# Kernel tuning notes

Hardware: AMD Instinct MI355X
Metric: run time of the kernel (lower is better)

The kernel has to match this reference:

```python
import jax, jax.numpy as jnp
import numpy as np

H, DST, DCONV, EXP = 640, 16, 4, 2
DIN = H * EXP          # 1280
DTR = -(-H // 16)      # 40
EPS = 1e-6


def rmsnorm(x, w):
    rms = jnp.sqrt(jnp.mean(x * x, axis=-1, keepdims=True) + EPS)
    return x / rms * w


def bitlinear(x, w, nw):
    # RMSNorm -> ternary weight quant + int8 activation quant (STE)
    x = rmsnorm(x, nw)
    alpha = jnp.maximum(jnp.mean(jnp.abs(w)), 1e-10)
    wq = jnp.clip(jnp.round(w / alpha), -1.0, 1.0)
    wq = w + jax.lax.stop_gradient(wq - w)
    gamma = jnp.maximum(jnp.max(jnp.abs(x), axis=-1, keepdims=True), 1e-10)
    xq = jnp.clip(jnp.round(x * 127.0 / gamma), -128.0, 127.0)
    xq = x + jax.lax.stop_gradient(xq - x)
    return (xq @ wq.T) * (alpha * gamma / 127.0)


def causal_conv1d(x, cw, cb):
    # x: [B,L,D]; depthwise causal conv, kernel DCONV
    pad = DCONV - 1
    xp = jnp.pad(x, ((0, 0), (pad, 0), (0, 0)))
    L = x.shape[1]
    out = jnp.zeros_like(x)
    for k in range(DCONV):
        out = out + xp[:, pad - k:pad - k + L, :] * cw[:, k]
    return out + cb


def selective_scan(x, dt, B_mat, C_mat, A_log):
    # x,dt: [B,L,D]; B_mat,C_mat: [B,L,N]; A_log: [D,N]
    A = -jnp.exp(A_log)
    dA = jnp.exp(A[None, None] * dt[..., None])                 # [B,L,D,N]
    dBx = dt[..., None] * B_mat[:, :, None, :] * x[..., None]   # [B,L,D,N]
    dA_t = jnp.moveaxis(dA, 1, 0)
    dBx_t = jnp.moveaxis(dBx, 1, 0)
    C_t = jnp.moveaxis(C_mat, 1, 0)

    def step(h, inp):
        da, dbx, c = inp
        h = da * h + dbx
        y = jnp.sum(h * c[:, None, :], axis=-1)  # [B,D]
        return h, y

    h0 = jnp.zeros(x.shape[:1] + (x.shape[2], A_log.shape[1]), x.dtype)
    _, ys = jax.lax.scan(step, h0, (dA_t, dBx_t, C_t))
    return jnp.moveaxis(ys, 0, 1)  # [B,L,D]


def setup_inputs() -> dict:
    key = jax.random.key(0)
    ks = jax.random.split(key, 10)
    sc_in = 1.0 / np.sqrt(H)
    sc_din = 1.0 / np.sqrt(DIN)
    A = np.tile(np.arange(1, DST + 1, dtype=np.float32)[None, :], (DIN, 1))
    return {
        "x": jax.random.normal(ks[0], (2, 2048, H), jnp.float32),
        "norm_w": jnp.ones((H,), jnp.float32),
        "in_w": jax.random.normal(ks[1], (DIN * 2, H), jnp.float32) * sc_in,
        "in_nw": jnp.ones((H,), jnp.float32),
        "conv_w": jax.random.normal(ks[2], (DIN, DCONV), jnp.float32) * 0.1,
        "conv_b": jnp.zeros((DIN,), jnp.float32),
        "dtu_w": jax.random.normal(ks[3], (DTR, DIN), jnp.float32) * sc_din,
        "dtu_nw": jnp.ones((DIN,), jnp.float32),
        "dtd_w": jax.random.normal(ks[4], (DIN, DTR), jnp.float32) / np.sqrt(DTR),
        "dtd_b": jnp.zeros((DIN,), jnp.float32),
        "Bp_w": jax.random.normal(ks[5], (DST, DIN), jnp.float32) * sc_din,
        "Bp_nw": jnp.ones((DIN,), jnp.float32),
        "Cp_w": jax.random.normal(ks[6], (DST, DIN), jnp.float32) * sc_din,
        "Cp_nw": jnp.ones((DIN,), jnp.float32),
        "A_log": jnp.asarray(np.log(A)),
        "D": jnp.ones((DIN,), jnp.float32),
        "out_w": jax.random.normal(ks[7], (H, DIN), jnp.float32) * sc_din,
        "out_nw": jnp.ones((DIN,), jnp.float32),
    }


def reference(x, norm_w, in_w, in_nw, conv_w, conv_b, dtu_w, dtu_nw, dtd_w, dtd_b,
              Bp_w, Bp_nw, Cp_w, Cp_nw, A_log, D, out_w, out_nw):
    residual = x
    xn = rmsnorm(x, norm_w)
    xz = bitlinear(xn, in_w, in_nw)
    x_path, z = jnp.split(xz, 2, axis=-1)
    x_path = causal_conv1d(x_path, conv_w, conv_b)
    x_path = jax.nn.silu(x_path)
    dt = jax.nn.softplus(bitlinear(x_path, dtu_w, dtu_nw) @ dtd_w.T + dtd_b)
    B_mat = bitlinear(x_path, Bp_w, Bp_nw)
    C_mat = bitlinear(x_path, Cp_w, Cp_nw)
    y = selective_scan(x_path, dt, B_mat, C_mat, A_log)
    y = y + x_path * D
    y = y * jax.nn.silu(z)
    return bitlinear(y, out_w, out_nw) + residual
```

## Files before the change

### kernel.cpp

```cpp
#include <hip/hip_runtime.h>
#include <hip/hip_bf16.h>
#include <cmath>

#define NROWS 4096
#define H_    640
#define DIN_  1280
#define DXZ   2560
#define DTR_  40
#define DST_  16
#define LSEQ  2048
#define EPS_  1e-6f
#define NCH   64
#define CL    32
#define NDG   20
#define KSPLIT 8
#define KCH (DIN_ / KSPLIT)
#define LOG2E 1.4426950408889634f
#define RLOG2E 0.6931471805599453f

typedef __attribute__((ext_vector_type(8))) short short8;
typedef __attribute__((ext_vector_type(4))) float f32x4;
typedef unsigned short ushort_t;

__device__ __forceinline__ float bf2f(short u) {
    return __uint_as_float((unsigned)(unsigned short)u << 16);
}
__device__ __forceinline__ short f2bfs(float x) { return (short)(__float_as_uint(x) >> 16); }

#define GLD16(gp, lp) __builtin_amdgcn_global_load_lds( \
    (const __attribute__((address_space(1))) unsigned int*)(unsigned long long)(gp), \
    (__attribute__((address_space(3))) unsigned int*)(unsigned int)(unsigned long long)(lp), 16, 0, 0)

__device__ __forceinline__ float wave_sum64(float v) {
    v += __shfl_xor(v, 1);  v += __shfl_xor(v, 2);  v += __shfl_xor(v, 4);
    v += __shfl_xor(v, 8);  v += __shfl_xor(v, 16); v += __shfl_xor(v, 32);
    return v;
}
__device__ __forceinline__ float wave_max64(float v) {
    v = fmaxf(v, __shfl_xor(v, 1));  v = fmaxf(v, __shfl_xor(v, 2));
    v = fmaxf(v, __shfl_xor(v, 4));  v = fmaxf(v, __shfl_xor(v, 8));
    v = fmaxf(v, __shfl_xor(v, 16)); v = fmaxf(v, __shfl_xor(v, 32));
    return v;
}
__device__ __forceinline__ float block_sum4(float v, float* red4) {
    v = wave_sum64(v);
    if ((threadIdx.x & 63) == 0) red4[threadIdx.x >> 6] = v;
    __syncthreads();
    return (red4[0] + red4[1]) + (red4[2] + red4[3]);
}
__device__ __forceinline__ float block_max4(float v, float* red4) {
    v = wave_max64(v);
    if ((threadIdx.x & 63) == 0) red4[threadIdx.x >> 6] = v;
    __syncthreads();
    return fmaxf(fmaxf(red4[0], red4[1]), fmaxf(red4[2], red4[3]));
}
__device__ __forceinline__ float block_reduce_sum256(float v, float* red) {
    int tid = threadIdx.x;
    red[tid] = v; __syncthreads();
    for (int o = 128; o; o >>= 1) { if (tid < o) red[tid] += red[tid + o]; __syncthreads(); }
    float r = red[0]; __syncthreads();
    return r;
}

__global__ __launch_bounds__(256) void k_pre(const float* __restrict__ x,
                                             const float* __restrict__ norm_w,
                                             const float* __restrict__ in_nw,
                                             const float* __restrict__ w0, const float* __restrict__ w1,
                                             const float* __restrict__ w2, const float* __restrict__ w3,
                                             const float* __restrict__ w4,
                                             int n0, int n1, int n2, int n3, int n4,
                                             __hip_bfloat16* __restrict__ xq, float* __restrict__ gamma,
                                             float* __restrict__ partials) {
    __shared__ float red[256];
    const int tid = threadIdx.x;
    if (blockIdx.x < NROWS) {
        const int r = blockIdx.x;
        const float* xr = x + (size_t)r * H_;
        const bool has2 = (tid < H_ - 512);
        float v0 = xr[tid], v1 = xr[tid + 256], v2 = has2 ? xr[tid + 512] : 0.f;
        float sum = block_sum4(v0 * v0 + v1 * v1 + v2 * v2, red);
        float r1 = 1.f / sqrtf(sum / H_ + EPS_);
        v0 *= r1 * norm_w[tid];
        v1 *= r1 * norm_w[tid + 256];
        if (has2) v2 *= r1 * norm_w[tid + 512];
        sum = block_sum4(v0 * v0 + v1 * v1 + v2 * v2, red + 4);
        float r2 = 1.f / sqrtf(sum / H_ + EPS_);
        v0 *= r2 * in_nw[tid];
        v1 *= r2 * in_nw[tid + 256];
        if (has2) v2 *= r2 * in_nw[tid + 512];
        float mx = fmaxf(fmaxf(fabsf(v0), fabsf(v1)), fabsf(v2));
        float g = fmaxf(block_max4(mx, red + 8), 1e-10f);
        if (tid == 0) gamma[r] = g;
        float s = 127.f / g;
        __hip_bfloat16* o = xq + (size_t)r * H_;
        o[tid]       = __float2bfloat16(fminf(fmaxf(rintf(v0 * s), -128.f), 127.f));
        o[tid + 256] = __float2bfloat16(fminf(fmaxf(rintf(v1 * s), -128.f), 127.f));
        if (has2) o[tid + 512] = __float2bfloat16(fminf(fmaxf(rintf(v2 * s), -128.f), 127.f));
    } else {
        const int flat = blockIdx.x - NROWS;
        const int wi = flat >> 8, xb = flat & 255;
        const float* w = (wi == 0) ? w0 : (wi == 1) ? w1 : (wi == 2) ? w2 : (wi == 3) ? w3 : w4;
        const int n = (wi == 0) ? n0 : (wi == 1) ? n1 : (wi == 2) ? n2 : (wi == 3) ? n3 : n4;
        float s = 0.f;
        for (int i = xb * 256 + tid; i < n; i += 65536) s += fabsf(w[i]);
        float t = block_reduce_sum256(s, red);
        if (tid == 0) partials[wi * 256 + xb] = t;
    }
}

__global__ __launch_bounds__(256) void absmean_final5(const float* __restrict__ partials,
                                                      int n0, int n1, int n2, int n3, int n4,
                                                      float* __restrict__ alphas) {
    const int wi = blockIdx.x;
    const int n = (wi == 0) ? n0 : (wi == 1) ? n1 : (wi == 2) ? n2 : (wi == 3) ? n3 : n4;
    __shared__ double red[256];
    double s = (double)partials[wi * 256 + threadIdx.x];
    red[threadIdx.x] = s; __syncthreads();
    for (int o = 128; o; o >>= 1) { if (threadIdx.x < o) red[threadIdx.x] += red[threadIdx.x + o]; __syncthreads(); }
    if (threadIdx.x == 0) alphas[wi] = fmaxf((float)(red[0] / (double)n), 1e-10f);
}

__global__ __launch_bounds__(256) void k_quant_build(const float* __restrict__ in_w,
                                                     const float* __restrict__ out_w,
                                                     const float* __restrict__ dtu_w,
                                                     const float* __restrict__ Bp_w,
                                                     const float* __restrict__ Cp_w,
                                                     const float* __restrict__ alphas,
                                                     __hip_bfloat16* __restrict__ q_in,
                                                     __hip_bfloat16* __restrict__ q_out,
                                                     ushort_t* __restrict__ wq_sk) {
    const int tid = threadIdx.x;
    if (blockIdx.x < 6400) {
        int i = blockIdx.x * 256 + tid;
        float a = alphas[0];
        ((ushort_t*)q_in)[i] = (ushort_t)f2bfs(fminf(fmaxf(rintf(in_w[i] / a), -1.f), 1.f));
    } else if (blockIdx.x < 9600) {
        int i = (blockIdx.x - 6400) * 256 + tid;
        float a = alphas[4];
        ((ushort_t*)q_out)[i] = (ushort_t)f2bfs(fminf(fmaxf(rintf(out_w[i] / a), -1.f), 1.f));
    } else {
        int idx = (blockIdx.x - 9600) * 256 + tid;
        int t = idx / 2560, rem = idx % 2560, kb = rem / 64, l = rem % 64;
        int nloc = l & 15, kg = l >> 4;
        float alpha; const float* src; int row; bool valid = true;
        if (t < 3)      { alpha = alphas[1]; src = dtu_w; row = t * 16 + nloc; valid = (row < 40); }
        else if (t == 3){ alpha = alphas[2]; src = Bp_w;  row = nloc; }
        else            { alpha = alphas[3]; src = Cp_w;  row = nloc; }
        int k0 = kb * 32 + kg * 8;
        short8 outv;
#pragma unroll
        for (int e = 0; e < 8; ++e) {
            float q = valid ? fminf(fmaxf(rintf(src[(size_t)row * DIN_ + k0 + e] / alpha), -1.f), 1.f) : 0.f;
            outv[e] = f2bfs(q);
        }
        *(short8*)(wq_sk + (size_t)idx * 8) = outv;
    }
}

template<int BM, int BN>
__global__ __launch_bounds__(256) void k_gemm_mfma(const ushort_t* __restrict__ Aq,
                                                   const ushort_t* __restrict__ Wq,
                                                   const float* __restrict__ alpha_p,
                                                   const float* __restrict__ gamma,
                                                   const float* __restrict__ residual,
                                                   float* __restrict__ out,
                                                   int M, int N, int K) {
    constexpr int FM = BM / 32, FN = BN / 32;
    constexpr int NL = (BM + BN) / 64;
    __shared__ ushort_t As[3][BM * 32];
    __shared__ ushort_t Bs[3][BN * 32];
    const int tid = threadIdx.x;
    const int w = tid >> 6, lane = tid & 63;
    const int wm = w >> 1, wn = w & 1;
    const int nwg = gridDim.x * gridDim.y;
    const int hw = blockIdx.y * gridDim.x + blockIdx.x;
    const int work = (nwg % 8 == 0) ? ((hw & 7) * (nwg >> 3) + (hw >> 3)) : hw;
    const int row0 = (work / gridDim.x) * BM;
    const int col0 = (work % gridDim.x) * BN;
    f32x4 acc[FM][FN] = {};

    auto stage = [&](int buf, int k0) {
        #pragma unroll
        for (int q = 0; q < BM / 64; ++q) {
            int c = w * BM + q * 64 + lane;
            int row = c >> 2;
            int uslot = (c & 3) ^ (row & 3);
            GLD16(Aq + (size_t)(row0 + row) * K + k0 + uslot * 8,
                  (char*)As[buf] + (w * BM + q * 64) * 16);
        }
        #pragma unroll
        for (int q = 0; q < BN / 64; ++q) {
            int c = w * BN + q * 64 + lane;
            int row = c >> 2;
            int uslot = (c & 3) ^ (row & 3);
            GLD16(Wq + (size_t)(col0 + row) * K + k0 + uslot * 8,
                  (char*)Bs[buf] + (w * BN + q * 64) * 16);
        }
    };

    const int NT = K >> 5;
    stage(0, 0);
    if (NT > 1) stage(1, 32);
    int cur = 0;
    for (int t = 0; t < NT; ++t) {
        if (t + 2 < NT) {
            int nb = cur + 2; if (nb >= 3) nb -= 3;
            stage(nb, (t + 2) << 5);
            if constexpr (NL == 2)      asm volatile("s_waitcnt vmcnt(4)" ::: "memory");
            else if constexpr (NL == 3) asm volatile("s_waitcnt vmcnt(6)" ::: "memory");
            else                        asm volatile("s_waitcnt vmcnt(8)" ::: "memory");
        } else if (t + 1 < NT) {
            if constexpr (NL == 2)      asm volatile("s_waitcnt vmcnt(2)" ::: "memory");
            else if constexpr (NL == 3) asm volatile("s_waitcnt vmcnt(3)" ::: "memory");
            else                        asm volatile("s_waitcnt vmcnt(4)" ::: "memory");
        } else {
            asm volatile("s_waitcnt vmcnt(0)" ::: "memory");
        }
        __builtin_amdgcn_s_barrier();

        short8 a[FM], b[FN];
        #pragma unroll
        for (int i = 0; i < FM; ++i) {
            int row = wm * (BM / 2) + i * 16 + (lane & 15);
            int byt = row * 64 + (((lane >> 4) ^ (row & 3)) << 4);
            a[i] = *(const short8*)((const char*)As[cur] + byt);
        }
        #pragma unroll
        for (int j = 0; j < FN; ++j) {
            int row = wn * (BN / 2) + j * 16 + (lane & 15);
            int byt = row * 64 + (((lane >> 4) ^ (row & 3)) << 4);
            b[j] = *(const short8*)((const char*)Bs[cur] + byt);
        }
        #pragma unroll
        for (int i = 0; i < FM; ++i)
            #pragma unroll
            for (int j = 0; j < FN; ++j)
                acc[i][j] = __builtin_amdgcn_mfma_f32_16x16x32_bf16(a[i], b[j], acc[i][j], 0, 0, 0);
        asm volatile("" ::: "memory");
        __builtin_amdgcn_s_barrier();
        ++cur; if (cur == 3) cur = 0;
    }

    const float alpha = alpha_p[0];
    #pragma unroll
    for (int i = 0; i < FM; ++i) {
        #pragma unroll
        for (int r = 0; r < 4; ++r) {
            int row = row0 + wm * (BM / 2) + i * 16 + (lane >> 4) * 4 + r;
            float s = alpha * gamma[row] * (1.f / 127.f);
            #pragma unroll
            for (int j = 0; j < FN; ++j) {
                int col = col0 + wn * (BN / 2) + j * 16 + (lane & 15);
                float o = acc[i][j][r] * s;
                if (residual) o += residual[(size_t)row * N + col];
                out[(size_t)row * N + col] = o;
            }
        }
    }
}

__global__ __launch_bounds__(256) void k_conv_norm(const float* __restrict__ xz,
                                                   const float* __restrict__ cw, const float* __restrict__ cb,
                                                   const float* __restrict__ dtu_nw,
                                                   const float* __restrict__ Bp_nw,
                                                   const float* __restrict__ Cp_nw,
                                                   float* __restrict__ xp,
                                                   float* __restrict__ rinv_out, float* __restrict__ g3) {
    const int row = blockIdx.x, tid = threadIdx.x;
    const int l = row & (LSEQ - 1);
    __shared__ float red4[16];
    float vv[5];
    float ss = 0.f;
#pragma unroll
    for (int j = 0; j < 5; ++j) {
        int d = tid + j * 256;
        f32x4 c4 = *(const f32x4*)(cw + (size_t)d * 4);
        const float* base = xz + (size_t)row * DXZ + d;
        float s = cb[d] + base[0] * c4[0];
        if (l >= 1) s += base[-(ptrdiff_t)DXZ] * c4[1];
        if (l >= 2) s += base[-(ptrdiff_t)(2 * DXZ)] * c4[2];
        if (l >= 3) s += base[-(ptrdiff_t)(3 * DXZ)] * c4[3];
        float v = s / (1.f + __builtin_amdgcn_exp2f(-s * LOG2E));
        vv[j] = v;
        ss += v * v;
        xp[(size_t)row * DIN_ + d] = v;
    }
    float sum = block_sum4(ss, red4);
    float rms = 1.f / sqrtf(sum / DIN_ + EPS_);
    float m0 = 0.f, m1 = 0.f, m2 = 0.f;
#pragma unroll
    for (int j = 0; j < 5; ++j) {
        int d = tid + j * 256;
        float t = vv[j] * rms;
        m0 = fmaxf(m0, fabsf(t * dtu_nw[d]));
        m1 = fmaxf(m1, fabsf(t * Bp_nw[d]));
        m2 = fmaxf(m2, fabsf(t * Cp_nw[d]));
    }
    float g0 = block_max4(m0, red4 + 4);
    float g1 = block_max4(m1, red4 + 8);
    float g2 = block_max4(m2, red4 + 12);
    if (tid == 0) {
        rinv_out[row]       = rms;
        g3[row]             = fmaxf(g0, 1e-10f);
        g3[NROWS + row]     = fmaxf(g1, 1e-10f);
        g3[2 * NROWS + row] = fmaxf(g2, 1e-10f);
    }
}

__global__ __launch_bounds__(256) void k_skinny_mfma(const float* __restrict__ xp,
                                                     const float* __restrict__ rinv,
                                                     const float* __restrict__ dtu_nw,
                                                     const float* __restrict__ Bp_nw,
                                                     const float* __restrict__ Cp_nw,
                                                     const float* __restrict__ g3,
                                                     const ushort_t* __restrict__ wq_sk,
                                                     float* __restrict__ dtu_acc,
                                                     float* __restrict__ B_acc,
                                                     float* __restrict__ C_acc) {
    const int tid = threadIdx.x;
    const int w = tid >> 6, l = tid & 63;
    const int row0 = blockIdx.x * 64;
    const int kc0 = blockIdx.y * KCH;
    __shared__ float s_xp[64 * 36];
    __shared__ float s_nw[3 * KCH];
    for (int i = tid; i < 3 * KCH; i += 256) {
        int m = i / KCH, j = i - m * KCH;
        const float* nw = (m == 0) ? dtu_nw : (m == 1) ? Bp_nw : Cp_nw;
        s_nw[i] = nw[kc0 + j];
    }
    const int arow = row0 + w * 16 + (l & 15);
    const float ri = rinv[arow];
    const float s0 = 127.f / g3[arow];
    const float s1 = 127.f / g3[NROWS + arow];
    const float s2 = 127.f / g3[2 * NROWS + arow];
    const int kgrp = l >> 4;
    f32x4 acc[5] = {};

    for (int ks = 0; ks < KCH / 32; ++ks) {
        const int kc = kc0 + ks * 32;
        __syncthreads();
        {
            int srow = tid >> 2, scol = (tid & 3) * 8;
            const float* gp = xp + (size_t)(row0 + srow) * DIN_ + kc + scol;
            f32x4 u0 = *(const f32x4*)gp;
            f32x4 u1 = *(const f32x4*)(gp + 4);
            *(f32x4*)(s_xp + srow * 36 + scol)     = u0;
            *(f32x4*)(s_xp + srow * 36 + scol + 4) = u1;
        }
        __syncthreads();
        const float* sp = s_xp + (w * 16 + (l & 15)) * 36 + kgrp * 8;
        f32x4 t0 = *(const f32x4*)sp;
        f32x4 t1 = *(const f32x4*)(sp + 4);
        float t[8] = { t0[0]*ri, t0[1]*ri, t0[2]*ri, t0[3]*ri,
                       t1[0]*ri, t1[1]*ri, t1[2]*ri, t1[3]*ri };
        short8 a0, a1, a2;
        #pragma unroll
        for (int e = 0; e < 8; ++e) {
            int kk = ks * 32 + kgrp * 8 + e;
            float q0 = fminf(fmaxf(rintf(t[e] * s_nw[kk]           * s0), -128.f), 127.f);
            float q1 = fminf(fmaxf(rintf(t[e] * s_nw[KCH + kk]     * s1), -128.f), 127.f);
            float q2 = fminf(fmaxf(rintf(t[e] * s_nw[2 * KCH + kk] * s2), -128.f), 127.f);
            a0[e] = f2bfs(q0); a1[e] = f2bfs(q1); a2[e] = f2bfs(q2);
        }
        const int kbg = kc >> 5;
        short8 b0 = *(const short8*)(wq_sk + ((size_t)(0 * 40 + kbg) * 64 + l) * 8);
        short8 b1 = *(const short8*)(wq_sk + ((size_t)(1 * 40 + kbg) * 64 + l) * 8);
        short8 b2 = *(const short8*)(wq_sk + ((size_t)(2 * 40 + kbg) * 64 + l) * 8);
        short8 b3 = *(const short8*)(wq_sk + ((size_t)(3 * 40 + kbg) * 64 + l) * 8);
        short8 b4 = *(const short8*)(wq_sk + ((size_t)(4 * 40 + kbg) * 64 + l) * 8);
        acc[0] = __builtin_amdgcn_mfma_f32_16x16x32_bf16(a0, b0, acc[0], 0, 0, 0);
        acc[1] = __builtin_amdgcn_mfma_f32_16x16x32_bf16(a0, b1, acc[1], 0, 0, 0);
        acc[2] = __builtin_amdgcn_mfma_f32_16x16x32_bf16(a0, b2, acc[2], 0, 0, 0);
        acc[3] = __builtin_amdgcn_mfma_f32_16x16x32_bf16(a1, b3, acc[3], 0, 0, 0);
        acc[4] = __builtin_amdgcn_mfma_f32_16x16x32_bf16(a2, b4, acc[4], 0, 0, 0);
    }

    const int col = l & 15;
    const int rbase = row0 + w * 16 + (l >> 4) * 4;
    #pragma unroll
    for (int j = 0; j < 4; ++j) {
        int r = rbase + j;
        atomicAdd(&dtu_acc[(size_t)r * DTR_ + col],      acc[0][j]);
        atomicAdd(&dtu_acc[(size_t)r * DTR_ + 16 + col], acc[1][j]);
        if (col < 8) atomicAdd(&dtu_acc[(size_t)r * DTR_ + 32 + col], acc[2][j]);
        atomicAdd(&B_acc[(size_t)r * DST_ + col], acc[3][j]);
        atomicAdd(&C_acc[(size_t)r * DST_ + col], acc[4][j]);
    }
}

__global__ __launch_bounds__(256) void k_dtd(const float* __restrict__ U,
                                             const float* __restrict__ W,
                                             const float* __restrict__ bias,
                                             const float* __restrict__ g3,
                                             const float* __restrict__ alphas,
                                             float* __restrict__ dt) {
    const int c0 = blockIdx.x * 64;
    const int r0 = blockIdx.y * 32;
    const int tid = threadIdx.x;
    const int col = tid & 63, rg = tid >> 6;
    __shared__ float s_w[64 * 41];
    __shared__ float s_u[32 * 40];
    for (int i = tid; i < 64 * 40; i += 256) {
        int cc = i / 40, t = i - cc * 40;
        s_w[cc * 41 + t] = W[(size_t)c0 * 40 + i];
    }
    const float alpha = alphas[1];
    for (int i = tid; i < 32 * 40; i += 256) {
        int rr = i / 40;
        s_u[i] = ((U[(size_t)r0 * 40 + i] * alpha) * g3[r0 + rr]) * (1.f / 127.f);
    }
    __syncthreads();
    float w[40];
#pragma unroll
    for (int t = 0; t < 40; t++) w[t] = s_w[col * 41 + t];
    const float b = bias[c0 + col];
    for (int r8 = 0; r8 < 8; ++r8) {
        const int row = rg * 8 + r8;
        const float* ur = s_u + row * 40;
        float a0 = b, a1 = 0.f, a2 = 0.f, a3 = 0.f;
#pragma unroll
        for (int t = 0; t < 40; t += 4) {
            f32x4 uv = *(const f32x4*)(ur + t);
            a0 = fmaf(uv[0], w[t],     a0);
            a1 = fmaf(uv[1], w[t + 1], a1);
            a2 = fmaf(uv[2], w[t + 2], a2);
            a3 = fmaf(uv[3], w[t + 3], a3);
        }
        float s = (a0 + a1) + (a2 + a3);
        float e = __builtin_amdgcn_exp2f(-fabsf(s) * LOG2E);
        float sp = fmaxf(s, 0.f) + __builtin_amdgcn_logf(1.f + e) * RLOG2E;
        dt[(size_t)(r0 + row) * DIN_ + c0 + col] = sp;
    }
}

__global__ __launch_bounds__(256) void k_scan_a(const float* __restrict__ dt, const float* __restrict__ xp,
                                                const float* __restrict__ Bm, const float* __restrict__ A_log,
                                                const float* __restrict__ g3, const float* __restrict__ alphas,
                                                float* __restrict__ hloc, float* __restrict__ sdt_out) {
    const int tid = threadIdx.x;
    const int q = tid & 3, dloc = tid >> 2;
    const int dg = blockIdx.x, c = blockIdx.y, b = blockIdx.z;
    const int d = dg * 64 + dloc;
    const int l0 = c * CL;
    __shared__ float s_B[CL * 16];
    if (tid < CL * 4) {
        int rg = b * LSEQ + l0 + (tid >> 2);
        float a2 = alphas[2];
        float gB = g3[NROWS + rg];
        f32x4 Bv = *(const f32x4*)(Bm + (size_t)rg * DST_ + (tid & 3) * 4);
        f32x4 o;
#pragma unroll
        for (int k = 0; k < 4; ++k) o[k] = ((Bv[k] * a2) * gB) * (1.f / 127.f);
        *(f32x4*)(s_B + tid * 4) = o;
    }
    f32x4 Av = *(const f32x4*)(A_log + (size_t)d * DST_ + q * 4);
    float A2[4];
#pragma unroll
    for (int j = 0; j < 4; ++j) A2[j] = -expf(Av[j]) * LOG2E;
    __syncthreads();
    const float* dtp = dt + (size_t)(b * LSEQ + l0) * DIN_ + d;
    const float* xpp = xp + (size_t)(b * LSEQ + l0) * DIN_ + d;
    float h[4] = {};
    float sdt = 0.f;
    float dtv = *dtp, xv = *xpp;
    for (int l = 0; l < CL; ++l) {
        float ndt = 0.f, nx = 0.f;
        if (l + 1 < CL) { ndt = dtp[(size_t)(l + 1) * DIN_]; nx = xpp[(size_t)(l + 1) * DIN_]; }
        f32x4 Bv = *(const f32x4*)(s_B + l * 16 + q * 4);
        float dtx = dtv * xv;
        sdt += dtv;
#pragma unroll
        for (int j = 0; j < 4; ++j) {
            float dA = __builtin_amdgcn_exp2f(A2[j] * dtv);
            h[j] = fmaf(dA, h[j], Bv[j] * dtx);
        }
        dtv = ndt; xv = nx;
    }
    size_t base = ((size_t)(b * NDG + dg) * 64 + c) * 1024 + tid * 4;
    *(f32x4*)(hloc + base) = (f32x4){h[0], h[1], h[2], h[3]};
    if (q == 0) sdt_out[((size_t)(b * NDG + dg) * 64 + c) * 64 + dloc] = sdt;
}

__global__ __launch_bounds__(256) void k_scan_b(float* __restrict__ hloc, const float* __restrict__ sdt,
                                                const float* __restrict__ A_log) {
    const int tid = threadIdx.x;
    const int idx = blockIdx.x;
    const int b = idx / (NDG * 64);
    const int rem = idx % (NDG * 64);
    const int dg = rem / 64, dloc = rem % 64;
    const int d = dg * 64 + dloc;
    __shared__ float s_h[64 * 17];
    __shared__ float s_sdt[64];
    __shared__ float s_A2[16];
    const size_t gb = (size_t)(b * NDG + dg) * 64;
#pragma unroll
    for (int i = 0; i < 4; ++i) {
        int c = i * 16 + (tid >> 4), n = tid & 15;
        s_h[c * 17 + n] = hloc[(gb + c) * 1024 + dloc * 16 + n];
    }
    if (tid < 64) s_sdt[tid] = sdt[(gb + tid) * 64 + dloc];
    else if (tid < 80) s_A2[tid - 64] = -expf(A_log[(size_t)d * DST_ + (tid - 64)]) * LOG2E;
    __syncthreads();
    const int w = tid >> 6, lane = tid & 63;
#pragma unroll
    for (int nn = 0; nn < 4; ++nn) {
        int n = w * 4 + nn;
        float h = s_h[lane * 17 + n];
        float P = __builtin_amdgcn_exp2f(s_A2[n] * s_sdt[lane]);
#pragma unroll
        for (int s = 1; s < 64; s <<= 1) {
            float hp = __shfl_up(h, s);
            float Pp = __shfl_up(P, s);
            if (lane >= s) { h = fmaf(P, hp, h); P *= Pp; }
        }
        float Hi = __shfl_up(h, 1);
        if (lane == 0) Hi = 0.f;
        s_h[lane * 17 + n] = Hi;
    }
    __syncthreads();
#pragma unroll
    for (int i = 0; i < 4; ++i) {
        int c = i * 16 + (tid >> 4), n = tid & 15;
        hloc[(gb + c) * 1024 + dloc * 16 + n] = s_h[c * 17 + n];
    }
}

__global__ __launch_bounds__(256) void k_scan_c(const float* __restrict__ dt, const float* __restrict__ xp,
                                                const float* __restrict__ Bm, const float* __restrict__ Cm,
                                                const float* __restrict__ xz, const float* __restrict__ A_log,
                                                const float* __restrict__ Dvec, const float* __restrict__ g3,
                                                const float* __restrict__ alphas,
                                                const float* __restrict__ Hinit, float* __restrict__ y) {
    const int tid = threadIdx.x;
    const int q = tid & 3, dloc = tid >> 2;
    const int dg = blockIdx.x, c = blockIdx.y, b = blockIdx.z;
    const int d = dg * 64 + dloc;
    const int l0 = c * CL;
    __shared__ float s_B[CL * 16], s_C[CL * 16];
    if (tid < CL * 4) {
        int rg = b * LSEQ + l0 + (tid >> 2);
        float a2 = alphas[2];
        float gB = g3[NROWS + rg];
        f32x4 Bv = *(const f32x4*)(Bm + (size_t)rg * DST_ + (tid & 3) * 4);
        f32x4 o;
#pragma unroll
        for (int k = 0; k < 4; ++k) o[k] = ((Bv[k] * a2) * gB) * (1.f / 127.f);
        *(f32x4*)(s_B + tid * 4) = o;
    } else {
        int t2 = tid - CL * 4;
        int rg = b * LSEQ + l0 + (t2 >> 2);
        float a3 = alphas[3];
        float gC = g3[2 * NROWS + rg];
        f32x4 Cv = *(const f32x4*)(Cm + (size_t)rg * DST_ + (t2 & 3) * 4);
        f32x4 o;
#pragma unroll
        for (int k = 0; k < 4; ++k) o[k] = ((Cv[k] * a3) * gC) * (1.f / 127.f);
        *(f32x4*)(s_C + t2 * 4) = o;
    }
    f32x4 Av = *(const f32x4*)(A_log + (size_t)d * DST_ + q * 4);
    float A2[4];
#pragma unroll
    for (int j = 0; j < 4; ++j) A2[j] = -expf(Av[j]) * LOG2E;
    const float Dd = Dvec[d];
    __syncthreads();
    const float* dtp = dt + (size_t)(b * LSEQ + l0) * DIN_ + d;
    const float* xpp = xp + (size_t)(b * LSEQ + l0) * DIN_ + d;
    const float* zp  = xz + (size_t)(b * LSEQ + l0) * DXZ + DIN_ + d;
    float* yp = y + (size_t)(b * LSEQ + l0) * DIN_ + d;
    size_t base = ((size_t)(b * NDG + dg) * 64 + c) * 1024 + tid * 4;
    f32x4 hv = *(const f32x4*)(Hinit + base);
    float h[4] = {hv[0], hv[1], hv[2], hv[3]};
    float dtv = *dtp, xv = *xpp, zv = *zp;
    for (int l = 0; l < CL; ++l) {
        float ndt = 0.f, nx = 0.f, nz = 0.f;
        if (l + 1 < CL) {
            ndt = dtp[(size_t)(l + 1) * DIN_];
            nx  = xpp[(size_t)(l + 1) * DIN_];
            nz  = zp[(size_t)(l + 1) * DXZ];
        }
        f32x4 Bv = *(const f32x4*)(s_B + l * 16 + q * 4);
        f32x4 Cv = *(const f32x4*)(s_C + l * 16 + q * 4);
        float dtx = dtv * xv;
        float yv = 0.f;
#pragma unroll
        for (int j = 0; j < 4; ++j) {
            float dA = __builtin_amdgcn_exp2f(A2[j] * dtv);
            h[j] = fmaf(dA, h[j], Bv[j] * dtx);
            yv = fmaf(h[j], Cv[j], yv);
        }
        yv += __shfl_xor(yv, 1);
        yv += __shfl_xor(yv, 2);
        if (q == 0) {
            float sig = 1.f / (1.f + __builtin_amdgcn_exp2f(-zv * LOG2E));
            yp[(size_t)l * DIN_] = (yv + xv * Dd) * (zv * sig);
        }
        dtv = ndt; xv = nx; zv = nz;
    }
}

__global__ __launch_bounds__(256) void k_norm_y(const float* __restrict__ y,
                                                const float* __restrict__ out_nw,
                                                __hip_bfloat16* __restrict__ yq, float* __restrict__ gy) {
    const int r = blockIdx.x, tid = threadIdx.x;
    const float* yr = y + (size_t)r * DIN_;
    __shared__ float red4[8];
    float v[5];
    float ss = 0.f;
#pragma unroll
    for (int j = 0; j < 5; j++) { v[j] = yr[tid + j * 256]; ss += v[j] * v[j]; }
    float sum = block_sum4(ss, red4);
    float rms = 1.f / sqrtf(sum / DIN_ + EPS_);
    float mx = 0.f;
#pragma unroll
    for (int j = 0; j < 5; j++) {
        int i = tid + j * 256;
        v[j] = v[j] * rms * out_nw[i];
        mx = fmaxf(mx, fabsf(v[j]));
    }
    float g = fmaxf(block_max4(mx, red4 + 4), 1e-10f);
    if (tid == 0) gy[r] = g;
    float s = 127.f / g;
#pragma unroll
    for (int j = 0; j < 5; j++) {
        int i = tid + j * 256;
        yq[(size_t)r * DIN_ + i] = __float2bfloat16(fminf(fmaxf(rintf(v[j] * s), -128.f), 127.f));
    }
}

extern "C" void kernel_launch(void* const* d_in, const int* in_sizes, int n_in,
                              void* d_out, int out_size, void* d_ws, size_t ws_size,
                              hipStream_t stream) {
    (void)in_sizes; (void)n_in; (void)out_size;
    const float* x      = (const float*)d_in[0];
    const float* norm_w = (const float*)d_in[1];
    const float* in_w   = (const float*)d_in[2];
    const float* in_nw  = (const float*)d_in[3];
    const float* conv_w = (const float*)d_in[4];
    const float* conv_b = (const float*)d_in[5];
    const float* dtu_w  = (const float*)d_in[6];
    const float* dtu_nw = (const float*)d_in[7];
    const float* dtd_w  = (const float*)d_in[8];
    const float* dtd_b  = (const float*)d_in[9];
    const float* Bp_w   = (const float*)d_in[10];
    const float* Bp_nw  = (const float*)d_in[11];
    const float* Cp_w   = (const float*)d_in[12];
    const float* Cp_nw  = (const float*)d_in[13];
    const float* A_log  = (const float*)d_in[14];
    const float* Dv     = (const float*)d_in[15];
    const float* out_w  = (const float*)d_in[16];
    const float* out_nw = (const float*)d_in[17];

    float* ws = (float*)d_ws;
    float* alphas   = ws;
    float* partials = ws + 8;
    float* xq1      = ws + 8 + 5 * 256;
    float* gamma1   = xq1 + (size_t)NROWS * H_;
    float* xz       = gamma1 + NROWS;
    float* xp       = xz + (size_t)NROWS * DXZ;
    float* xpn     = xp + (size_t)NROWS * DIN_;
    float* g3       = xpn + (size_t)NROWS * DIN_;
    float* dtu_out  = g3 + 3 * NROWS;
    float* Bmat     = dtu_out + (size_t)NROWS * DTR_;
    float* Cmat     = Bmat + (size_t)NROWS * DST_;
    float* dtb      = Cmat + (size_t)NROWS * DST_;
    float* gy       = dtb + (size_t)NROWS * DIN_;
    float* wq_in    = gy + NROWS;
    float* wq_dtu   = wq_in + (size_t)DXZ * H_;
    float* wq_Bp    = wq_dtu + (size_t)DTR_ * DIN_;
    float* wq_Cp    = wq_Bp + (size_t)DST_ * DIN_;
    float* wq_out   = wq_Cp + (size_t)DST_ * DIN_;
    float* rinv     = wq_out + (size_t)H_ * DIN_;
    float* wq_sk    = rinv + NROWS;
    float* sdt      = wq_sk + 51200;
    size_t need = (size_t)((sdt + 2 * NDG * 64 * 64) - ws) * sizeof(float);
    if (ws_size < need) return;

    float* hloc = xq1;

    hipMemsetAsync(dtu_out, 0, (size_t)NROWS * 72 * sizeof(float), stream);

    const int n0 = DXZ * H_, n1 = DTR_ * DIN_, n2 = DST_ * DIN_, n3 = DST_ * DIN_, n4 = H_ * DIN_;
    hipLaunchKernelGGL(k_pre, dim3(NROWS + 5 * 256), dim3(256), 0, stream,
                       x, norm_w, in_nw, in_w, dtu_w, Bp_w, Cp_w, out_w,
                       n0, n1, n2, n3, n4, (__hip_bfloat16*)xq1, gamma1, partials);
    hipLaunchKernelGGL(absmean_final5, dim3(5), dim3(256), 0, stream, partials, n0, n1, n2, n3, n4, alphas);
    hipLaunchKernelGGL(k_quant_build, dim3(9650), dim3(256), 0, stream,
                       in_w, out_w, dtu_w, Bp_w, Cp_w, alphas,
                       (__hip_bfloat16*)wq_in, (__hip_bfloat16*)wq_out, (ushort_t*)wq_sk);

    hipLaunchKernelGGL((k_gemm_mfma<128, 128>), dim3(DXZ / 128, NROWS / 128), dim3(256), 0, stream,
                       (const ushort_t*)xq1, (const ushort_t*)wq_in, alphas + 0, gamma1,
                       (const float*)nullptr, xz, NROWS, DXZ, H_);
    hipLaunchKernelGGL(k_conv_norm, dim3(NROWS), dim3(256), 0, stream,
                       xz, conv_w, conv_b, dtu_nw, Bp_nw, Cp_nw, xp, rinv, g3);
    hipLaunchKernelGGL(k_skinny_mfma, dim3(NROWS / 64, KSPLIT), dim3(256), 0, stream,
                       xp, rinv, dtu_nw, Bp_nw, Cp_nw, g3, (const ushort_t*)wq_sk,
                       dtu_out, Bmat, Cmat);
    hipLaunchKernelGGL(k_dtd, dim3(DIN_ / 64, NROWS / 32), dim3(256), 0, stream,
                       dtu_out, dtd_w, dtd_b, g3, alphas, dtb);

    hipLaunchKernelGGL(k_scan_a, dim3(NDG, NCH, 2), dim3(256), 0, stream,
                       dtb, xp, Bmat, A_log, g3, alphas, hloc, sdt);
    hipLaunchKernelGGL(k_scan_b, dim3(2 * NDG * 64), dim3(256), 0, stream, hloc, sdt, A_log);
    hipLaunchKernelGGL(k_scan_c, dim3(NDG, NCH, 2), dim3(256), 0, stream,
                       dtb, xp, Bmat, Cmat, xz, A_log, Dv, g3, alphas, hloc, xpn );

    hipLaunchKernelGGL(k_norm_y, dim3(NROWS), dim3(256), 0, stream, xpn , out_nw,
                       (__hip_bfloat16*)dtb , gy);
    hipLaunchKernelGGL((k_gemm_mfma<64, 64>), dim3(H_ / 64, NROWS / 64), dim3(256), 0, stream,
                       (const ushort_t*)dtb , (const ushort_t*)wq_out, alphas + 4, gy,
                       x , (float*)d_out, NROWS, H_, DIN_);
}
```

Baseline: 226.9 us.

## Fold memset and absmean finalize into neighbouring kernels; remap conv row order

Drops the separate hipMemsetAsync by zeroing the split-K accumulator inside k_pre's weight-reduction blocks. Drops the absmean_final5 launch by having every k_quant_build block reduce the 256 partials itself to get its alpha, with block 0 writing all five alphas for later kernels. Also permutes the row-to-block mapping in k_conv_norm, interleaving blocks across sequence positions. The aim is fewer launches and less serialization, at the cost of redundant per-block double-precision reductions and extra syncs in the quant kernel.

```diff
diff --git a/kernel.cpp b/kernel.cpp
--- a/kernel.cpp
+++ b/kernel.cpp
@@ -70,7 +70,8 @@
                                              const float* __restrict__ w4,
                                              int n0, int n1, int n2, int n3, int n4,
                                              __hip_bfloat16* __restrict__ xq, float* __restrict__ gamma,
-                                             float* __restrict__ partials) {
+                                             float* __restrict__ partials,
+                                             float* __restrict__ zacc ) {
     __shared__ float red[256];
     const int tid = threadIdx.x;
     if (blockIdx.x < NROWS) {
@@ -98,6 +99,7 @@
         if (has2) o[tid + 512] = __float2bfloat16(fminf(fmaxf(rintf(v2 * s), -128.f), 127.f));
     } else {
         const int flat = blockIdx.x - NROWS;
+        for (int i = flat * 256 + tid; i < NROWS * 72; i += 1280 * 256) zacc[i] = 0.f;
         const int wi = flat >> 8, xb = flat & 255;
         const float* w = (wi == 0) ? w0 : (wi == 1) ? w1 : (wi == 2) ? w2 : (wi == 3) ? w3 : w4;
         const int n = (wi == 0) ? n0 : (wi == 1) ? n1 : (wi == 2) ? n2 : (wi == 3) ? n3 : n4;
@@ -108,44 +110,51 @@
     }
 }
 
-__global__ __launch_bounds__(256) void absmean_final5(const float* __restrict__ partials,
-                                                      int n0, int n1, int n2, int n3, int n4,
-                                                      float* __restrict__ alphas) {
-    const int wi = blockIdx.x;
-    const int n = (wi == 0) ? n0 : (wi == 1) ? n1 : (wi == 2) ? n2 : (wi == 3) ? n3 : n4;
-    __shared__ double red[256];
-    double s = (double)partials[wi * 256 + threadIdx.x];
-    red[threadIdx.x] = s; __syncthreads();
-    for (int o = 128; o; o >>= 1) { if (threadIdx.x < o) red[threadIdx.x] += red[threadIdx.x + o]; __syncthreads(); }
-    if (threadIdx.x == 0) alphas[wi] = fmaxf((float)(red[0] / (double)n), 1e-10f);
-}
-
 __global__ __launch_bounds__(256) void k_quant_build(const float* __restrict__ in_w,
                                                      const float* __restrict__ out_w,
                                                      const float* __restrict__ dtu_w,
                                                      const float* __restrict__ Bp_w,
                                                      const float* __restrict__ Cp_w,
-                                                     const float* __restrict__ alphas,
+                                                     const float* __restrict__ partials,
+                                                     float* __restrict__ alphas,
                                                      __hip_bfloat16* __restrict__ q_in,
                                                      __hip_bfloat16* __restrict__ q_out,
-                                                     ushort_t* __restrict__ wq_sk) {
-    const int tid = threadIdx.x;
+                                                     ushort_t* __restrict__ wq_sk,
+                                                     int n0, int n1, int n2, int n3, int n4) {
+    __shared__ double dred[256];
+    const int tid = threadIdx.x;
+    auto calc_alpha = [&](int wi, int n) -> float {
+        double s = (double)partials[wi * 256 + tid];
+        dred[tid] = s; __syncthreads();
+        for (int o = 128; o; o >>= 1) { if (tid < o) dred[tid] += dred[tid + o]; __syncthreads(); }
+        float a = fmaxf((float)(dred[0] / (double)n), 1e-10f);
+        __syncthreads();
+        return a;
+    };
     if (blockIdx.x < 6400) {
+        float a = calc_alpha(0, n0);
+        if (blockIdx.x == 0) {
+            float a1 = calc_alpha(1, n1), a2 = calc_alpha(2, n2);
+            float a3 = calc_alpha(3, n3), a4 = calc_alpha(4, n4);
+            if (tid == 0) {
+                alphas[0] = a; alphas[1] = a1; alphas[2] = a2; alphas[3] = a3; alphas[4] = a4;
+            }
+        }
         int i = blockIdx.x * 256 + tid;
-        float a = alphas[0];
         ((ushort_t*)q_in)[i] = (ushort_t)f2bfs(fminf(fmaxf(rintf(in_w[i] / a), -1.f), 1.f));
     } else if (blockIdx.x < 9600) {
+        float a = calc_alpha(4, n4);
         int i = (blockIdx.x - 6400) * 256 + tid;
-        float a = alphas[4];
         ((ushort_t*)q_out)[i] = (ushort_t)f2bfs(fminf(fmaxf(rintf(out_w[i] / a), -1.f), 1.f));
     } else {
+        float a1 = calc_alpha(1, n1), a2 = calc_alpha(2, n2), a3 = calc_alpha(3, n3);
         int idx = (blockIdx.x - 9600) * 256 + tid;
         int t = idx / 2560, rem = idx % 2560, kb = rem / 64, l = rem % 64;
         int nloc = l & 15, kg = l >> 4;
         float alpha; const float* src; int row; bool valid = true;
-        if (t < 3)      { alpha = alphas[1]; src = dtu_w; row = t * 16 + nloc; valid = (row < 40); }
-        else if (t == 3){ alpha = alphas[2]; src = Bp_w;  row = nloc; }
-        else            { alpha = alphas[3]; src = Cp_w;  row = nloc; }
+        if (t < 3)      { alpha = a1; src = dtu_w; row = t * 16 + nloc; valid = (row < 40); }
+        else if (t == 3){ alpha = a2; src = Bp_w;  row = nloc; }
+        else            { alpha = a3; src = Cp_w;  row = nloc; }
         int k0 = kb * 32 + kg * 8;
         short8 outv;
 #pragma unroll
@@ -266,7 +275,9 @@
                                                    const float* __restrict__ Cp_nw,
                                                    float* __restrict__ xp,
                                                    float* __restrict__ rinv_out, float* __restrict__ g3) {
-    const int row = blockIdx.x, tid = threadIdx.x;
+    const int bb = blockIdx.x;
+    const int row = ((bb & 7) << 9) | (bb >> 3);
+    const int tid = threadIdx.x;
     const int l = row & (LSEQ - 1);
     __shared__ float red4[16];
     float vv[5];
@@ -677,16 +688,14 @@
 
     float* hloc = xq1;
 
-    hipMemsetAsync(dtu_out, 0, (size_t)NROWS * 72 * sizeof(float), stream);
-
     const int n0 = DXZ * H_, n1 = DTR_ * DIN_, n2 = DST_ * DIN_, n3 = DST_ * DIN_, n4 = H_ * DIN_;
     hipLaunchKernelGGL(k_pre, dim3(NROWS + 5 * 256), dim3(256), 0, stream,
                        x, norm_w, in_nw, in_w, dtu_w, Bp_w, Cp_w, out_w,
-                       n0, n1, n2, n3, n4, (__hip_bfloat16*)xq1, gamma1, partials);
-    hipLaunchKernelGGL(absmean_final5, dim3(5), dim3(256), 0, stream, partials, n0, n1, n2, n3, n4, alphas);
+                       n0, n1, n2, n3, n4, (__hip_bfloat16*)xq1, gamma1, partials, dtu_out);
     hipLaunchKernelGGL(k_quant_build, dim3(9650), dim3(256), 0, stream,
-                       in_w, out_w, dtu_w, Bp_w, Cp_w, alphas,
-                       (__hip_bfloat16*)wq_in, (__hip_bfloat16*)wq_out, (ushort_t*)wq_sk);
+                       in_w, out_w, dtu_w, Bp_w, Cp_w, partials, alphas,
+                       (__hip_bfloat16*)wq_in, (__hip_bfloat16*)wq_out, (ushort_t*)wq_sk,
+                       n0, n1, n2, n3, n4);
 
     hipLaunchKernelGGL((k_gemm_mfma<128, 128>), dim3(DXZ / 128, NROWS / 128), dim3(256), 0, stream,
                        (const ushort_t*)xq1, (const ushort_t*)wq_in, alphas + 0, gamma1,
```

Result: no change. 223.6 us (-1.5%).
